# Performance work log

Hardware: AMD Instinct MI355X
Metric: run time of the kernel (lower is better)

The kernel has to match this reference:

```python
import jax, jax.numpy as jnp
import numpy as np

H = 768            # hidden_size
I = 384            # moe_intermediate_size
E = 16             # n_routed_experts
G = 4              # n_group
TOPK_GROUP = 2
TOP_K = 4
SCALE = 2.5        # routed_scaling_factor
N_SHARED = 2
IS = I * N_SHARED  # shared expert intermediate
B, S = 1, 2048


def setup_inputs() -> dict:
    key = jax.random.key(0)
    ks = jax.random.split(key, 16)
    s = lambda k, shape, fan: jax.random.normal(k, shape, jnp.float32) * (fan ** -0.5)
    return {
        'hidden_states': jax.random.normal(ks[0], (B, S, H), jnp.float32),
        # router
        'router_w': s(ks[1], (E, H), H),
        'router_b': jnp.zeros((E,), jnp.float32),
        'corr_bias': jnp.zeros((E,), jnp.float32),
        # routed experts, stacked [E, ...]
        'gWg': s(ks[2], (E, H, I), H),
        'gbg': jnp.zeros((E, I), jnp.float32),
        'gWu': s(ks[3], (E, H, I), H),
        'gbu': jnp.zeros((E, I), jnp.float32),
        'gWd': s(ks[4], (E, I, H), I),
        'gbd': jnp.zeros((E, H), jnp.float32),
        # shared expert
        'sWg': s(ks[5], (H, IS), H),
        'sbg': jnp.zeros((IS,), jnp.float32),
        'sWu': s(ks[6], (H, IS), H),
        'sbu': jnp.zeros((IS,), jnp.float32),
        'sWd': s(ks[7], (IS, H), IS),
        'sbd': jnp.zeros((H,), jnp.float32),
    }


def _route(x, router_w, router_b, corr_bias):
    # x: [T, H] -> topk_indices [T, K], topk_weights [T, K]
    logits = x.astype(jnp.float32) @ router_w.T + router_b          # [T, E]
    scores = jax.nn.sigmoid(logits)
    sfc = scores + corr_bias[None, :]                                # [T, E]
    # group scores: sum of top-2 per group
    grp = sfc.reshape(-1, G, E // G)
    group_scores = jax.lax.top_k(grp, 2)[0].sum(-1)                  # [T, G]
    _, gidx = jax.lax.top_k(group_scores, TOPK_GROUP)                # [T, topk_group]
    gmask = jax.nn.one_hot(gidx, G, dtype=sfc.dtype).sum(axis=1)     # [T, G]
    score_mask = jnp.repeat(gmask, E // G, axis=-1)                  # [T, E]
    sfc = jnp.where(score_mask > 0, sfc, 0.0)
    _, idx = jax.lax.top_k(sfc, TOP_K)                               # [T, K]
    w = jnp.take_along_axis(scores, idx, axis=1)                     # [T, K]
    w = w / (w.sum(-1, keepdims=True) + 1e-20)                       # norm_topk_prob
    return idx, w * SCALE


def reference(hidden_states, router_w, router_b, corr_bias,
              gWg, ggbg, gWu, gbu, gWd, gbd,
              sWg, sbg, sWu, sbu, sWd, sbd):
    # note: arg name gbg kept consistent below
    return _forward(hidden_states, router_w, router_b, corr_bias,
                    gWg, gbg_fix(gWg, gbg := gbg_dummy()), gWu, gbu, gWd, gbd,
                    sWg, sbg, sWu, sbu, sWd, sbd)


# --- real implementation (the above placeholder is replaced here) ---

def _forward(x3, router_w, router_b, corr_bias, gWg, gbg, gWu, gbu, gWd, gbd,
             sWg, sbg, sWu, sbu, sWd, sbd):
    orig_shape = x3.shape
    x = x3.reshape(-1, H)                                            # [T, H]
    idx, w = _route(x, router_w, router_b, corr_bias)
    # combine weights per (token, expert): zero for non-selected experts
    c = (jax.nn.one_hot(idx, E, dtype=w.dtype) * w[..., None]).sum(1)  # [T, E]
    # all-expert gated MLP (zero combine weight => zero contribution)
    h = jax.nn.silu(jnp.einsum('th,ehi->tei', x, gWg) + gbg) * \
        (jnp.einsum('th,ehi->tei', x, gWu) + gbu)                    # [T, E, I]
    out_e = jnp.einsum('tei,eih->teh', h, gWd) + gbd                 # [T, E, H]
    moe_out = jnp.einsum('te,teh->th', c, out_e)                     # [T, H]
    # shared experts on the residual input
    hs = jax.nn.silu(x @ sWg + sbg) * (x @ sWu + sbu)
    shared = hs @ sWd + sbd
    return (moe_out + shared).reshape(orig_shape)


def reference(hidden_states, router_w, router_b, corr_bias,
              gWg, gbg, gWu, gbu, gWd, gbd,
              sWg, sbg, sWu, sbu, sWd, sbd):
    return _forward(hidden_states, router_w, router_b, corr_bias,
                    gWg, gbg, gWu, gbu, gWd, gbd,
                    sWg, sbg, sWu, sbu, sWd, sbd)
```

## Files before the change

kernel.cpp:

```cpp
#include <hip/hip_runtime.h>
#include <hip/hip_bf16.h>
#include <math.h>

#define H 768
#define I_DIM 384
#define E_NUM 16
#define G_NUM 4
#define TOPK 4
#define IS_DIM 768
#define SCALE_F 2.5f

#define BM 128
#define BK 32
#define LDA 40

typedef __attribute__((ext_vector_type(8))) __bf16 bf16x8;
typedef __attribute__((ext_vector_type(4))) float f32x4;

static __device__ __forceinline__ unsigned short f2bf(float f) {
    __bf16 h = (__bf16)f;
    return __builtin_bit_cast(unsigned short, h);
}

static __device__ __forceinline__ int swz8(int row, int c) {
    return row * LDA + (((c ^ (row >> 3)) & 3) << 3);
}

__global__ __launch_bounds__(256) void router_score_k(
    const float* __restrict__ X, const float* __restrict__ RW,
    const float* __restrict__ RB, const float* __restrict__ CB,
    int* __restrict__ sel_out, float* __restrict__ w_out,
    unsigned short* __restrict__ Xb, int T)
{
    const int wid = threadIdx.x >> 6;
    const int lane = threadIdx.x & 63;
    const int t = blockIdx.x * 4 + wid;
    const int e = lane & 15;
    const int chunk = lane >> 4;
    const float* xr = X + (size_t)t * H + chunk * (H / 4);
    const float* wr = RW + (size_t)e * H + chunk * (H / 4);
    float s = 0.f;
#pragma unroll 4
    for (int j = 0; j < H / 4; j += 4) {
        float4 a = *(const float4*)(xr + j);
        float4 b = *(const float4*)(wr + j);
        s += a.x * b.x + a.y * b.y + a.z * b.z + a.w * b.w;
    }
    s += __shfl_xor(s, 16);
    s += __shfl_xor(s, 32);

    {
        const float* xrow = X + (size_t)t * H;
        unsigned short* brow = Xb + (size_t)t * H;
#pragma unroll
        for (int p = 0; p < 3; ++p) {
            float4 v = *(const float4*)(xrow + p * 256 + lane * 4);
            ushort4 o = { f2bf(v.x), f2bf(v.y), f2bf(v.z), f2bf(v.w) };
            *(ushort4*)(brow + p * 256 + lane * 4) = o;
        }
    }

    __shared__ float sc_s[4][E_NUM];
    __shared__ float sf_s[4][E_NUM];
    if (lane < E_NUM) {
        float logit = s + RB[e];
        float score = 1.f / (1.f + expf(-logit));
        sc_s[wid][e] = score;
        sf_s[wid][e] = score + CB[e];
    }
    __syncthreads();

    if (lane == 0) {
        float gs[G_NUM];
        for (int g = 0; g < G_NUM; ++g) {
            float m1 = -1e30f, m2 = -1e30f;
            for (int j = 0; j < E_NUM / G_NUM; ++j) {
                float v = sf_s[wid][g * (E_NUM / G_NUM) + j];
                if (v > m1) { m2 = m1; m1 = v; }
                else if (v > m2) { m2 = v; }
            }
            gs[g] = m1 + m2;
        }
        int g1 = 0;
        for (int g = 1; g < G_NUM; ++g) if (gs[g] > gs[g1]) g1 = g;
        int g2 = -1;
        for (int g = 0; g < G_NUM; ++g) {
            if (g == g1) continue;
            if (g2 < 0 || gs[g] > gs[g2]) g2 = g;
        }
        float m[E_NUM];
        for (int i = 0; i < E_NUM; ++i) {
            int g = i >> 2;
            m[i] = (g == g1 || g == g2) ? sf_s[wid][i] : 0.f;
        }
        float wsum = 0.f;
        int sel[TOPK]; float wv[TOPK];
        for (int k = 0; k < TOPK; ++k) {
            int best = 0; float bv = -1e30f;
            for (int i = 0; i < E_NUM; ++i)
                if (m[i] > bv) { bv = m[i]; best = i; }
            m[best] = -2e30f;
            sel[k] = best;
            wv[k] = sc_s[wid][best];
            wsum += wv[k];
        }
        float inv = SCALE_F / (wsum + 1e-20f);
        int4 so = { sel[0], sel[1], sel[2], sel[3] };
        float4 wo = { wv[0] * inv, wv[1] * inv, wv[2] * inv, wv[3] * inv };
        *(int4*)&sel_out[(size_t)t * 4] = so;
        *(float4*)&w_out[(size_t)t * 4] = wo;
    }
}

__global__ __launch_bounds__(256) void build_lists_k(
    const int* __restrict__ sel, const float* __restrict__ wv,
    int* __restrict__ cnt, int* __restrict__ tok_id, float* __restrict__ tok_w,
    int T)
{
    const int e = blockIdx.x;
    const int tid = threadIdx.x;
    const int wid = tid >> 6, lane = tid & 63;
    __shared__ int wtot[4];
    __shared__ int base_s;
    if (tid == 0) base_s = 0;
    __syncthreads();

    for (int t0 = 0; t0 < T; t0 += 256) {
        const int t = t0 + tid;
        int flag = 0; float myw = 0.f;
        int4 sv = *(const int4*)&sel[(size_t)t * 4];
        float4 wq = *(const float4*)&wv[(size_t)t * 4];
        if (sv.x == e) { flag = 1; myw = wq.x; }
        if (sv.y == e) { flag = 1; myw = wq.y; }
        if (sv.z == e) { flag = 1; myw = wq.z; }
        if (sv.w == e) { flag = 1; myw = wq.w; }
        unsigned long long mb = __ballot(flag);
        if (lane == 0) wtot[wid] = __popcll(mb);
        __syncthreads();
        int wo = 0;
#pragma unroll
        for (int q = 0; q < 4; ++q) if (q < wid) wo += wtot[q];
        const int stot = wtot[0] + wtot[1] + wtot[2] + wtot[3];
        const int mypos = base_s + wo + __popcll(mb & ((1ull << lane) - 1ull));
        if (flag) {
            tok_id[(size_t)e * T + mypos] = t;
            tok_w[(size_t)e * T + mypos] = myw;
        }
        __syncthreads();
        if (tid == 0) base_s += stot;
    }
    __syncthreads();
    if (tid == 0) cnt[e] = base_s;
}

__global__ void scan_k(const int* __restrict__ cnt, int* __restrict__ offs)
{
    if (threadIdx.x == 0) {
        int a = 0;
        for (int e2 = 0; e2 < E_NUM; ++e2) { offs[e2] = a; a += cnt[e2]; }
        offs[E_NUM] = a;
    }
}

static __device__ __forceinline__ void wr4(
    unsigned short* Bt, int n, int kr, float4 v)
{
    const int cg = kr >> 3, kl = kr & 7;
    Bt[(n + 0) * LDA + (((cg ^ ((n + 0) >> 3)) & 3) << 3) + kl] = f2bf(v.x);
    Bt[(n + 1) * LDA + (((cg ^ ((n + 1) >> 3)) & 3) << 3) + kl] = f2bf(v.y);
    Bt[(n + 2) * LDA + (((cg ^ ((n + 2) >> 3)) & 3) << 3) + kl] = f2bf(v.z);
    Bt[(n + 3) * LDA + (((cg ^ ((n + 3) >> 3)) & 3) << 3) + kl] = f2bf(v.w);
}

__global__ __launch_bounds__(256) void gateup_all_k(
    const unsigned short* __restrict__ Xb,
    const float* __restrict__ GWg, const float* __restrict__ GWu,
    const float* __restrict__ Gbg, const float* __restrict__ Gbu,
    const float* __restrict__ SWg, const float* __restrict__ SWu,
    const float* __restrict__ Sbg, const float* __restrict__ Sbu,
    const int* __restrict__ cnt, const int* __restrict__ offs,
    const int* __restrict__ tok_id,
    unsigned short* __restrict__ HBr,
    unsigned short* __restrict__ HSs,
    int T)
{
    const int z = blockIdx.z;
    const bool SH = (z == E_NUM);
    const int NI = SH ? IS_DIM : I_DIM;
    const int n0 = blockIdx.y * 64;
    if (n0 >= NI) return;
    const int ne = SH ? T : cnt[z];
    const int m0 = blockIdx.x * BM;
    if (m0 >= ne) return;

    const float* Wg = SH ? SWg : GWg + (size_t)z * H * I_DIM;
    const float* Wu = SH ? SWu : GWu + (size_t)z * H * I_DIM;
    const float* bg = SH ? Sbg : Gbg + z * I_DIM;
    const float* bu = SH ? Sbu : Gbu + z * I_DIM;
    unsigned short* HO = SH ? HSs : HBr;
    const int obase = SH ? 0 : offs[z];
    const int* tl = tok_id + (size_t)z * T;

    __shared__ unsigned short Al[BM * LDA];
    __shared__ unsigned short Bgl[64 * LDA];
    __shared__ unsigned short Bul[64 * LDA];

    const int tid = threadIdx.x;
    const int srow = tid >> 2;
    const int sseg = (tid & 3) * 8;
    const int kr0 = tid >> 4;
    const int c4 = (tid & 15) * 4;

    int r0i = m0 + srow, r1i = m0 + srow + 64;
    if (!SH) { r0i = min(r0i, ne - 1); r1i = min(r1i, ne - 1); }
    const int tok0 = SH ? r0i : tl[r0i];
    const int tok1 = SH ? r1i : tl[r1i];
    const unsigned short* a0p = Xb + (size_t)tok0 * H + sseg;
    const unsigned short* a1p = Xb + (size_t)tok1 * H + sseg;

    const int lane = tid & 63;
    const int wvid = tid >> 6;
    const int wr = wvid >> 1, wc = wvid & 1;
    const int lrow = lane & 15;
    const int lkc = lane >> 4;

    f32x4 accg[4][2] = {};
    f32x4 accu[4][2] = {};

    uint4 av0, av1; float4 gv0, gv1, uv0, uv1;
#define GU_LOADS(K)                                                        \
    av0 = *(const uint4*)(a0p + (K));                                      \
    av1 = *(const uint4*)(a1p + (K));                                      \
    gv0 = *(const float4*)(Wg + (size_t)((K) + kr0) * NI + n0 + c4);       \
    gv1 = *(const float4*)(Wg + (size_t)((K) + kr0 + 16) * NI + n0 + c4);  \
    uv0 = *(const float4*)(Wu + (size_t)((K) + kr0) * NI + n0 + c4);       \
    uv1 = *(const float4*)(Wu + (size_t)((K) + kr0 + 16) * NI + n0 + c4);

    GU_LOADS(0);
    for (int k0 = 0; k0 < H; k0 += BK) {
        __syncthreads();
        *(uint4*)&Al[swz8(srow, tid & 3)] = av0;
        *(uint4*)&Al[swz8(srow + 64, tid & 3)] = av1;
        wr4(Bgl, c4, kr0, gv0);
        wr4(Bgl, c4, kr0 + 16, gv1);
        wr4(Bul, c4, kr0, uv0);
        wr4(Bul, c4, kr0 + 16, uv1);
        __syncthreads();
        if (k0 + BK < H) { GU_LOADS(k0 + BK); }
        bf16x8 af[4], gf[2], uf[2];
#pragma unroll
        for (int i = 0; i < 4; ++i)
            af[i] = *(const bf16x8*)&Al[swz8(wr * 64 + i * 16 + lrow, lkc)];
#pragma unroll
        for (int j = 0; j < 2; ++j) {
            gf[j] = *(const bf16x8*)&Bgl[swz8(wc * 32 + j * 16 + lrow, lkc)];
            uf[j] = *(const bf16x8*)&Bul[swz8(wc * 32 + j * 16 + lrow, lkc)];
        }
#pragma unroll
        for (int i = 0; i < 4; ++i)
#pragma unroll
            for (int j = 0; j < 2; ++j) {
                accg[i][j] = __builtin_amdgcn_mfma_f32_16x16x32_bf16(af[i], gf[j], accg[i][j], 0, 0, 0);
                accu[i][j] = __builtin_amdgcn_mfma_f32_16x16x32_bf16(af[i], uf[j], accu[i][j], 0, 0, 0);
            }
    }
#undef GU_LOADS

    const int q4 = (lane >> 4) * 4;
    const int cc = lane & 15;
#pragma unroll
    for (int i = 0; i < 4; ++i)
#pragma unroll
        for (int j = 0; j < 2; ++j)
#pragma unroll
            for (int r = 0; r < 4; ++r) {
                const int row = m0 + wr * 64 + i * 16 + q4 + r;
                if (SH || row < ne) {
                    const int col = n0 + wc * 32 + j * 16 + cc;
                    float g = accg[i][j][r] + bg[col];
                    float u = accu[i][j][r] + bu[col];
                    float s = g / (1.f + expf(-g)) * u;
                    HO[(size_t)(obase + row) * NI + col] = f2bf(s);
                }
            }
}

template<bool SCATTER>
__global__ __launch_bounds__(256) void down_mfma_k(
    const unsigned short* __restrict__ Hb,
    const float* __restrict__ WdP,
    const float* __restrict__ bdp,
    const int* __restrict__ cnt, const int* __restrict__ offs,
    const int* __restrict__ tok_id, const float* __restrict__ tok_w,
    float* __restrict__ OUT, int T, int K)
{
    const int e = SCATTER ? blockIdx.z : 0;
    const int ne = SCATTER ? cnt[e] : T;
    const int m0 = blockIdx.x * BM;
    if (m0 >= ne) return;
    const int n0 = blockIdx.y * 128;

    const float* Wd = WdP + (SCATTER ? (size_t)e * K * H : 0);
    const float* bd = bdp + (SCATTER ? e * H : 0);
    const int abase = SCATTER ? offs[e] : 0;

    __shared__ unsigned short Al[BM * LDA];
    __shared__ unsigned short Bl[128 * LDA];

    const int tid = threadIdx.x;
    const int srow = tid >> 2;
    const int sseg = (tid & 3) * 8;
    const int kr0 = tid >> 5;
    const int c4 = (tid & 31) * 4;

    const int r0i = min(m0 + srow, ne - 1);
    const int r1i = min(m0 + srow + 64, ne - 1);
    const unsigned short* a0p = Hb + (size_t)(abase + r0i) * K + sseg;
    const unsigned short* a1p = Hb + (size_t)(abase + r1i) * K + sseg;

    const int lane = tid & 63;
    const int wvid = tid >> 6;
    const int wr = wvid >> 1, wc = wvid & 1;
    const int lrow = lane & 15;
    const int lkc = lane >> 4;

    f32x4 acc[4][4] = {};

    uint4 av0, av1; float4 bv0, bv1, bv2, bv3;
#define DN_LOADS(K0)                                                        \
    av0 = *(const uint4*)(a0p + (K0));                                      \
    av1 = *(const uint4*)(a1p + (K0));                                      \
    bv0 = *(const float4*)(Wd + (size_t)((K0) + kr0) * H + n0 + c4);        \
    bv1 = *(const float4*)(Wd + (size_t)((K0) + kr0 + 8) * H + n0 + c4);    \
    bv2 = *(const float4*)(Wd + (size_t)((K0) + kr0 + 16) * H + n0 + c4);   \
    bv3 = *(const float4*)(Wd + (size_t)((K0) + kr0 + 24) * H + n0 + c4);

    DN_LOADS(0);
    for (int k0 = 0; k0 < K; k0 += BK) {
        __syncthreads();
        *(uint4*)&Al[swz8(srow, tid & 3)] = av0;
        *(uint4*)&Al[swz8(srow + 64, tid & 3)] = av1;
        wr4(Bl, c4, kr0, bv0);
        wr4(Bl, c4, kr0 + 8, bv1);
        wr4(Bl, c4, kr0 + 16, bv2);
        wr4(Bl, c4, kr0 + 24, bv3);
        __syncthreads();
        if (k0 + BK < K) { DN_LOADS(k0 + BK); }
        bf16x8 af[4], bfr[4];
#pragma unroll
        for (int i = 0; i < 4; ++i) {
            af[i]  = *(const bf16x8*)&Al[swz8(wr * 64 + i * 16 + lrow, lkc)];
            bfr[i] = *(const bf16x8*)&Bl[swz8(wc * 64 + i * 16 + lrow, lkc)];
        }
#pragma unroll
        for (int i = 0; i < 4; ++i)
#pragma unroll
            for (int j = 0; j < 4; ++j)
                acc[i][j] = __builtin_amdgcn_mfma_f32_16x16x32_bf16(af[i], bfr[j], acc[i][j], 0, 0, 0);
    }
#undef DN_LOADS

    const int q4 = (lane >> 4) * 4;
    const int cc = lane & 15;
#pragma unroll
    for (int i = 0; i < 4; ++i) {
        const int rbase = m0 + wr * 64 + i * 16 + q4;
        if (SCATTER) {
#pragma unroll
            for (int r = 0; r < 4; ++r) {
                const int row = rbase + r;
                if (row < ne) {
                    const int tok = tok_id[(size_t)e * T + row];
                    const float w = tok_w[(size_t)e * T + row];
#pragma unroll
                    for (int j = 0; j < 4; ++j) {
                        const int col = n0 + wc * 64 + j * 16 + cc;
                        atomicAdd(&OUT[(size_t)tok * H + col], w * (acc[i][j][r] + bd[col]));
                    }
                }
            }
        } else {
#pragma unroll
            for (int r = 0; r < 4; ++r) {
                const int row = rbase + r;
#pragma unroll
                for (int j = 0; j < 4; ++j) {
                    const int col = n0 + wc * 64 + j * 16 + cc;
                    OUT[(size_t)row * H + col] = acc[i][j][r] + bd[col];
                }
            }
        }
    }
}

extern "C" void kernel_launch(void* const* d_in, const int* in_sizes, int n_in,
                              void* d_out, int out_size, void* d_ws, size_t ws_size,
                              hipStream_t stream)
{
    const float* X   = (const float*)d_in[0];
    const float* RW  = (const float*)d_in[1];
    const float* RB  = (const float*)d_in[2];
    const float* CB  = (const float*)d_in[3];
    const float* GWg = (const float*)d_in[4];
    const float* Gbg = (const float*)d_in[5];
    const float* GWu = (const float*)d_in[6];
    const float* Gbu = (const float*)d_in[7];
    const float* GWd = (const float*)d_in[8];
    const float* Gbd = (const float*)d_in[9];
    const float* SWg = (const float*)d_in[10];
    const float* Sbg = (const float*)d_in[11];
    const float* SWu = (const float*)d_in[12];
    const float* Sbu = (const float*)d_in[13];
    const float* SWd = (const float*)d_in[14];
    const float* Sbd = (const float*)d_in[15];
    float* OUT = (float*)d_out;
    const int T = in_sizes[0] / H;

    char* w = (char*)d_ws;
    int* cnt     = (int*)w;            w += 256;
    int* offs    = (int*)w;            w += 256;
    int* sel     = (int*)w;            w += (size_t)T * TOPK * sizeof(int);
    float* selw  = (float*)w;          w += (size_t)T * TOPK * sizeof(float);
    int* tok_id  = (int*)w;            w += (size_t)E_NUM * T * sizeof(int);
    float* tok_w = (float*)w;          w += (size_t)E_NUM * T * sizeof(float);
    unsigned short* Xb  = (unsigned short*)w; w += (size_t)T * H * 2;
    unsigned short* HSs = (unsigned short*)w; w += (size_t)T * IS_DIM * 2;
    unsigned short* HBr = (unsigned short*)w; w += (size_t)T * TOPK * I_DIM * 2;

    router_score_k<<<T / 4, 256, 0, stream>>>(X, RW, RB, CB, sel, selw, Xb, T);
    build_lists_k<<<E_NUM, 256, 0, stream>>>(sel, selw, cnt, tok_id, tok_w, T);
    scan_k<<<1, 64, 0, stream>>>(cnt, offs);

    gateup_all_k<<<dim3(T / BM, IS_DIM / 64, E_NUM + 1), 256, 0, stream>>>(
        Xb, GWg, GWu, Gbg, Gbu, SWg, SWu, Sbg, Sbu,
        cnt, offs, tok_id, HBr, HSs, T);

    down_mfma_k<false><<<dim3(T / BM, H / 128, 1), 256, 0, stream>>>(
        HSs, SWd, Sbd, nullptr, nullptr, nullptr, nullptr, OUT, T, IS_DIM);

    down_mfma_k<true><<<dim3(T / BM, H / 128, E_NUM), 256, 0, stream>>>(
        HBr, GWd, Gbd, cnt, offs, tok_id, tok_w, OUT, T, I_DIM);
}
```

Before: 347.4 us.

## Merge shared and routed down-projections into one launch with XCD-aware block swizzle

Replaces the two down-projection launches (shared dense store plus routed atomic scatter) with a single kernel covering all 17 expert slots. The output is zeroed with a memset and the shared expert now accumulates through atomics. Both gate/up and down kernels switch to a 1D grid whose index is decoded so that each 8-way XCD stripe covers 16 M-tiles of the same (expert, N-tile) group, aiming at better L2 reuse of weight tiles. The cost is an extra memset and extra atomic traffic for the shared-expert rows.

```diff
diff --git a/kernel.cpp b/kernel.cpp
--- a/kernel.cpp
+++ b/kernel.cpp
@@ -172,6 +172,16 @@
     Bt[(n + 3) * LDA + (((cg ^ ((n + 3) >> 3)) & 3) << 3) + kl] = f2bf(v.w);
 }
 
+static __device__ __forceinline__ bool decode_swz(
+    int p, int GTOT, int& x, int& g)
+{
+    const int xcd = p & 7;
+    const int rem = p >> 3;
+    x = rem & 15;
+    g = xcd + 8 * (rem >> 4);
+    return g < GTOT;
+}
+
 __global__ __launch_bounds__(256) void gateup_all_k(
     const unsigned short* __restrict__ Xb,
     const float* __restrict__ GWg, const float* __restrict__ GWu,
@@ -184,13 +194,15 @@
     unsigned short* __restrict__ HSs,
     int T)
 {
-    const int z = blockIdx.z;
+    int x, g;
+    if (!decode_swz(blockIdx.x, 12 * (E_NUM + 1), x, g)) return;
+    const int y = g % 12, z = g / 12;
     const bool SH = (z == E_NUM);
     const int NI = SH ? IS_DIM : I_DIM;
-    const int n0 = blockIdx.y * 64;
+    const int n0 = y * 64;
     if (n0 >= NI) return;
     const int ne = SH ? T : cnt[z];
-    const int m0 = blockIdx.x * BM;
+    const int m0 = x * BM;
     if (m0 >= ne) return;
 
     const float* Wg = SH ? SWg : GWg + (size_t)z * H * I_DIM;
@@ -277,32 +289,37 @@
                 const int row = m0 + wr * 64 + i * 16 + q4 + r;
                 if (SH || row < ne) {
                     const int col = n0 + wc * 32 + j * 16 + cc;
-                    float g = accg[i][j][r] + bg[col];
+                    float gq = accg[i][j][r] + bg[col];
                     float u = accu[i][j][r] + bu[col];
-                    float s = g / (1.f + expf(-g)) * u;
+                    float s = gq / (1.f + expf(-gq)) * u;
                     HO[(size_t)(obase + row) * NI + col] = f2bf(s);
                 }
             }
 }
 
-template<bool SCATTER>
-__global__ __launch_bounds__(256) void down_mfma_k(
-    const unsigned short* __restrict__ Hb,
-    const float* __restrict__ WdP,
-    const float* __restrict__ bdp,
+__global__ __launch_bounds__(256) void down_all_k(
+    const unsigned short* __restrict__ HBr,
+    const unsigned short* __restrict__ HSs,
+    const float* __restrict__ GWd, const float* __restrict__ Gbd,
+    const float* __restrict__ SWd, const float* __restrict__ Sbd,
     const int* __restrict__ cnt, const int* __restrict__ offs,
     const int* __restrict__ tok_id, const float* __restrict__ tok_w,
-    float* __restrict__ OUT, int T, int K)
-{
-    const int e = SCATTER ? blockIdx.z : 0;
-    const int ne = SCATTER ? cnt[e] : T;
-    const int m0 = blockIdx.x * BM;
+    float* __restrict__ OUT, int T)
+{
+    int x, g;
+    if (!decode_swz(blockIdx.x, 6 * (E_NUM + 1), x, g)) return;
+    const int y = g % 6, z = g / 6;
+    const bool SH = (z == E_NUM);
+    const int ne = SH ? T : cnt[z];
+    const int m0 = x * BM;
     if (m0 >= ne) return;
-    const int n0 = blockIdx.y * 128;
-
-    const float* Wd = WdP + (SCATTER ? (size_t)e * K * H : 0);
-    const float* bd = bdp + (SCATTER ? e * H : 0);
-    const int abase = SCATTER ? offs[e] : 0;
+    const int n0 = y * 128;
+    const int K = SH ? IS_DIM : I_DIM;
+
+    const float* Wd = SH ? SWd : GWd + (size_t)z * I_DIM * H;
+    const float* bd = SH ? Sbd : Gbd + (size_t)z * H;
+    const unsigned short* Hb = SH ? HSs : HBr;
+    const int abase = SH ? 0 : offs[z];
 
     __shared__ unsigned short Al[BM * LDA];
     __shared__ unsigned short Bl[128 * LDA];
@@ -365,28 +382,22 @@
 #pragma unroll
     for (int i = 0; i < 4; ++i) {
         const int rbase = m0 + wr * 64 + i * 16 + q4;
-        if (SCATTER) {
-#pragma unroll
-            for (int r = 0; r < 4; ++r) {
-                const int row = rbase + r;
-                if (row < ne) {
-                    const int tok = tok_id[(size_t)e * T + row];
-                    const float w = tok_w[(size_t)e * T + row];
-#pragma unroll
-                    for (int j = 0; j < 4; ++j) {
-                        const int col = n0 + wc * 64 + j * 16 + cc;
-                        atomicAdd(&OUT[(size_t)tok * H + col], w * (acc[i][j][r] + bd[col]));
-                    }
-                }
-            }
-        } else {
-#pragma unroll
-            for (int r = 0; r < 4; ++r) {
-                const int row = rbase + r;
+#pragma unroll
+        for (int r = 0; r < 4; ++r) {
+            const int row = rbase + r;
+            if (SH) {
 #pragma unroll
                 for (int j = 0; j < 4; ++j) {
                     const int col = n0 + wc * 64 + j * 16 + cc;
-                    OUT[(size_t)row * H + col] = acc[i][j][r] + bd[col];
+                    atomicAdd(&OUT[(size_t)row * H + col], acc[i][j][r] + bd[col]);
+                }
+            } else if (row < ne) {
+                const int tok = tok_id[(size_t)z * T + row];
+                const float w = tok_w[(size_t)z * T + row];
+#pragma unroll
+                for (int j = 0; j < 4; ++j) {
+                    const int col = n0 + wc * 64 + j * 16 + cc;
+                    atomicAdd(&OUT[(size_t)tok * H + col], w * (acc[i][j][r] + bd[col]));
                 }
             }
         }
@@ -427,17 +438,16 @@
     unsigned short* HSs = (unsigned short*)w; w += (size_t)T * IS_DIM * 2;
     unsigned short* HBr = (unsigned short*)w; w += (size_t)T * TOPK * I_DIM * 2;
 
+    hipMemsetAsync(OUT, 0, (size_t)out_size * sizeof(float), stream);
+
     router_score_k<<<T / 4, 256, 0, stream>>>(X, RW, RB, CB, sel, selw, Xb, T);
     build_lists_k<<<E_NUM, 256, 0, stream>>>(sel, selw, cnt, tok_id, tok_w, T);
     scan_k<<<1, 64, 0, stream>>>(cnt, offs);
 
-    gateup_all_k<<<dim3(T / BM, IS_DIM / 64, E_NUM + 1), 256, 0, stream>>>(
+    gateup_all_k<<<3328, 256, 0, stream>>>(
         Xb, GWg, GWu, Gbg, Gbu, SWg, SWu, Sbg, Sbu,
         cnt, offs, tok_id, HBr, HSs, T);
 
-    down_mfma_k<false><<<dim3(T / BM, H / 128, 1), 256, 0, stream>>>(
-        HSs, SWd, Sbd, nullptr, nullptr, nullptr, nullptr, OUT, T, IS_DIM);
-
-    down_mfma_k<true><<<dim3(T / BM, H / 128, E_NUM), 256, 0, stream>>>(
-        HBr, GWd, Gbd, cnt, offs, tok_id, tok_w, OUT, T, I_DIM);
-}
+    down_all_k<<<1664, 256, 0, stream>>>(
+        HBr, HSs, GWd, Gbd, SWd, Sbd, cnt, offs, tok_id, tok_w, OUT, T);
+}
```

Result: faster. 292.4 us (-15.8%).
